# Optimization experiments

Measured on AMD Instinct MI355X. Metric: run time of the kernel, lower is better.

## Reference

```python
import jax, jax.numpy as jnp
import numpy as np

EPS = 1e-5

def batchnorm(x, gamma, beta):
    # training-mode BatchNorm1d: biased batch stats over axis 0
    mu = jnp.mean(x, axis=0)
    var = jnp.var(x, axis=0)
    return (x - mu) * jax.lax.rsqrt(var + EPS) * gamma + beta

def setup_inputs() -> dict:
    key = jax.random.key(0)
    ks = jax.random.split(key, 8)
    N, E, Hn, He = 50000, 800000, 128, 128
    node_emb = jax.random.normal(ks[0], (N, Hn), dtype=jnp.float32)
    edge_emb = jax.random.normal(ks[1], (E, He), dtype=jnp.float32)
    i = jax.random.randint(ks[2], (E,), 0, N, dtype=jnp.int64)
    fan_in = Hn + He
    W1 = jax.random.normal(ks[3], (fan_in, 2 * Hn), dtype=jnp.float32) / np.sqrt(fan_in)
    b1 = jnp.zeros((2 * Hn,), dtype=jnp.float32)
    gamma1 = jnp.ones((2 * Hn,), dtype=jnp.float32)
    beta1 = jnp.zeros((2 * Hn,), dtype=jnp.float32)
    gamma2 = jnp.ones((Hn,), dtype=jnp.float32)
    beta2 = jnp.zeros((Hn,), dtype=jnp.float32)
    return {"node_emb": node_emb, "edge_emb": edge_emb, "i": i,
            "W1": W1, "b1": b1, "gamma1": gamma1, "beta1": beta1,
            "gamma2": gamma2, "beta2": beta2}

def reference(node_emb, edge_emb, i, W1, b1, gamma1, beta1, gamma2, beta2):
    N = node_emb.shape[0]
    # gather + concat: [E, Hn+He]
    c1 = jnp.concatenate([node_emb[i], edge_emb], axis=1)
    # linear + BN: [E, 2*Hn]
    c1 = batchnorm(c1 @ W1 + b1, gamma1, beta1)
    c1_filter, c1_core = jnp.split(c1, 2, axis=1)
    msg = jax.nn.sigmoid(c1_filter) * jnp.tanh(c1_core)  # gated: [E, Hn]
    agg = jax.ops.segment_sum(msg, i, num_segments=N)     # scatter-add: [N, Hn]
    c1_emb = batchnorm(agg, gamma2, beta2)
    return jnp.tanh(node_emb + c1_emb)
```

## Files before the change

### kernel.cpp

```cpp
#include <hip/hip_runtime.h>
#include <hip/hip_bf16.h>

typedef __attribute__((ext_vector_type(8))) short short8;
typedef __attribute__((ext_vector_type(4))) float f32x4;

#define EPS 1e-5f

__device__ inline unsigned short bf16_rne(float x) {
    unsigned u = __float_as_uint(x);
    unsigned r = u + 0x7FFFu + ((u >> 16) & 1u);
    return (unsigned short)(r >> 16);
}

__device__ inline float sigmoidf_fast(float x) {
    return 1.0f / (1.0f + __expf(-x));
}

__device__ inline float tanhf_fast(float x) {
    float ax = fabsf(x);
    float e = __expf(-2.0f * ax);
    float t = (1.0f - e) / (1.0f + e);
    return copysignf(t, x);
}

__global__ void prep_w(const float* __restrict__ W1,
                       short* __restrict__ WhiT, short* __restrict__ WloT) {
    int n = blockIdx.x;
    int k = threadIdx.x;
    float x = W1[k * 256 + n];
    unsigned short hi = bf16_rne(x);
    float fh = __uint_as_float(((unsigned)hi) << 16);
    unsigned short lo = bf16_rne(x - fh);
    WhiT[n * 256 + k] = (short)hi;
    WloT[n * 256 + k] = (short)lo;
}

__global__ __launch_bounds__(256) void gemm_stats(
    const float* __restrict__ node_emb, const float* __restrict__ edge_emb,
    const int* __restrict__ idx,
    const short* __restrict__ WhiT, const short* __restrict__ WloT,
    const float* __restrict__ b1, float* __restrict__ h,
    float* __restrict__ sum1, float* __restrict__ sumsq1) {
    __shared__ __align__(16) short Ahi[64 * 128];
    __shared__ __align__(16) short Alo[64 * 128];

    const int tid = threadIdx.x;
    const int row0 = blockIdx.x * 64;
    const int r = tid >> 2;
    const int q = tid & 3;
    const size_t e = (size_t)row0 + r;
    const float* nodeptr = node_emb + (size_t)idx[e] * 128;
    const float* edgeptr = edge_emb + e * 128;

    const int lane = tid & 63;
    const int wid = tid >> 6;
    const int l15 = lane & 15;
    const int lg = lane >> 4;

    f32x4 acc[4][4];
#pragma unroll
    for (int a = 0; a < 4; ++a)
#pragma unroll
        for (int b = 0; b < 4; ++b) acc[a][b] = (f32x4){0.f, 0.f, 0.f, 0.f};

    const short* bbase_hi = WhiT + (wid * 64 + l15) * 256 + lg * 8;
    const short* bbase_lo = WloT + (wid * 64 + l15) * 256 + lg * 8;

#pragma unroll
    for (int ph = 0; ph < 2; ++ph) {
        const float* src = ph ? edgeptr : nodeptr;
        if (ph) __syncthreads();
#pragma unroll
        for (int cc = 0; cc < 4; ++cc) {
            const int c = q * 4 + cc;
            const int k0 = c * 8;
            float4 va = *(const float4*)(src + k0);
            float4 vb = *(const float4*)(src + k0 + 4);
            float vals[8] = {va.x, va.y, va.z, va.w, vb.x, vb.y, vb.z, vb.w};
            short8 vhi, vlo;
#pragma unroll
            for (int j = 0; j < 8; ++j) {
                unsigned short hb = bf16_rne(vals[j]);
                float fh = __uint_as_float(((unsigned)hb) << 16);
                unsigned short lb = bf16_rne(vals[j] - fh);
                vhi[j] = (short)hb;
                vlo[j] = (short)lb;
            }
            const int off = r * 128 + (c ^ (r & 7)) * 8;
            *(short8*)(Ahi + off) = vhi;
            *(short8*)(Alo + off) = vlo;
        }
        __syncthreads();

#pragma unroll
        for (int ks = 0; ks < 4; ++ks) {
            short8 ah[4], al[4];
#pragma unroll
            for (int mt = 0; mt < 4; ++mt) {
                const int row = mt * 16 + l15;
                const int off = row * 128 + ((ks * 4 + lg) ^ (row & 7)) * 8;
                ah[mt] = *(const short8*)(Ahi + off);
                al[mt] = *(const short8*)(Alo + off);
            }
            const int kglob = ph * 128 + ks * 32;
#pragma unroll
            for (int nt = 0; nt < 4; ++nt) {
                short8 bh = *(const short8*)(bbase_hi + nt * 16 * 256 + kglob);
                short8 bl = *(const short8*)(bbase_lo + nt * 16 * 256 + kglob);
#pragma unroll
                for (int mt = 0; mt < 4; ++mt) {
                    acc[mt][nt] = __builtin_amdgcn_mfma_f32_16x16x32_bf16(
                        ah[mt], bh, acc[mt][nt], 0, 0, 0);
                    acc[mt][nt] = __builtin_amdgcn_mfma_f32_16x16x32_bf16(
                        ah[mt], bl, acc[mt][nt], 0, 0, 0);
                    acc[mt][nt] = __builtin_amdgcn_mfma_f32_16x16x32_bf16(
                        al[mt], bh, acc[mt][nt], 0, 0, 0);
                }
            }
        }
    }

    const int colbase = wid * 64 + l15;
#pragma unroll
    for (int nt = 0; nt < 4; ++nt) {
        const int col = colbase + nt * 16;
        const float bv = b1[col];
        float s = 0.f, qq = 0.f;
#pragma unroll
        for (int mt = 0; mt < 4; ++mt) {
            const size_t rbase = (size_t)row0 + mt * 16 + lg * 4;
#pragma unroll
            for (int v = 0; v < 4; ++v) {
                float hv = acc[mt][nt][v] + bv;
                h[(rbase + v) * 256 + col] = hv;
                s += hv;
                qq += hv * hv;
            }
        }
        s += __shfl_xor(s, 16);
        s += __shfl_xor(s, 32);
        qq += __shfl_xor(qq, 16);
        qq += __shfl_xor(qq, 32);
        if (lg == 0) {
            atomicAdd(&sum1[col], s);
            atomicAdd(&sumsq1[col], qq);
        }
    }
}

__global__ void bn1_finalize(const float* __restrict__ sum1,
                             const float* __restrict__ sumsq1,
                             const float* __restrict__ gamma1,
                             const float* __restrict__ beta1,
                             float* __restrict__ s1t1, int E) {
    int c = threadIdx.x;
    float invE = 1.0f / (float)E;
    float mu = sum1[c] * invE;
    float var = sumsq1[c] * invE - mu * mu;
    float s = gamma1[c] * rsqrtf(var + EPS);
    s1t1[c] = s;
    s1t1[256 + c] = beta1[c] - mu * s;
}

__global__ void csr_hist(const int* __restrict__ idx, int* __restrict__ cnt,
                         int E) {
    int e = blockIdx.x * 256 + threadIdx.x;
    if (e < E) atomicAdd(&cnt[idx[e]], 1);
}

__global__ __launch_bounds__(1024) void csr_scan(const int* __restrict__ cnt,
                                                 int* __restrict__ offs, int N) {
    __shared__ int part[1024];
    const int t = threadIdx.x;
    const int CH = (N + 1023) / 1024;
    const int base = t * CH;
    int s = 0;
    for (int i = 0; i < CH; ++i)
        if (base + i < N) s += cnt[base + i];
    part[t] = s;
    __syncthreads();
    for (int d = 1; d < 1024; d <<= 1) {
        int v = (t >= d) ? part[t - d] : 0;
        __syncthreads();
        part[t] += v;
        __syncthreads();
    }
    int run = (t ? part[t - 1] : 0);
    for (int i = 0; i < CH; ++i) {
        int g = base + i;
        if (g < N) {
            offs[g] = run;
            run += cnt[g];
        }
    }
    if (t == 1023) offs[N] = run;
}

__global__ void csr_fill(const int* __restrict__ idx,
                         const int* __restrict__ offs, int* __restrict__ cursor,
                         int* __restrict__ elist, int E) {
    int e = blockIdx.x * 256 + threadIdx.x;
    if (e < E) {
        int n = idx[e];
        int p = atomicAdd(&cursor[n], 1);
        elist[offs[n] + p] = e;
    }
}

__global__ __launch_bounds__(256) void gate_gather(
    const float* __restrict__ h, const int* __restrict__ offs,
    const int* __restrict__ elist, const float* __restrict__ s1t1,
    float* __restrict__ agg, int N) {
    const int t = threadIdx.x;
    const int n = blockIdx.x * 8 + (t >> 5);
    const int c = (t & 31) * 4;
    const float4 sf = *(const float4*)(s1t1 + c);
    const float4 tf = *(const float4*)(s1t1 + 256 + c);
    const float4 sc = *(const float4*)(s1t1 + 128 + c);
    const float4 tc = *(const float4*)(s1t1 + 384 + c);
    const int j0 = offs[n];
    const int j1 = offs[n + 1];
    float a0 = 0.f, a1 = 0.f, a2 = 0.f, a3 = 0.f;
    for (int j = j0; j < j1; ++j) {
        const size_t e = (size_t)elist[j];
        const float4 hf = *(const float4*)(h + e * 256 + c);
        const float4 hc = *(const float4*)(h + e * 256 + 128 + c);
        a0 += sigmoidf_fast(hf.x * sf.x + tf.x) * tanhf_fast(hc.x * sc.x + tc.x);
        a1 += sigmoidf_fast(hf.y * sf.y + tf.y) * tanhf_fast(hc.y * sc.y + tc.y);
        a2 += sigmoidf_fast(hf.z * sf.z + tf.z) * tanhf_fast(hc.z * sc.z + tc.z);
        a3 += sigmoidf_fast(hf.w * sf.w + tf.w) * tanhf_fast(hc.w * sc.w + tc.w);
    }
    *(float4*)(agg + (size_t)n * 128 + c) = make_float4(a0, a1, a2, a3);
}

__global__ void bn2_stats(const float* __restrict__ agg, float* __restrict__ sum2,
                          float* __restrict__ sumsq2, int N) {
    const int gt = blockIdx.x * blockDim.x + threadIdx.x;
    const int c = (gt & 31) * 4;
    int r = gt >> 5;
    const int rstride = (gridDim.x * blockDim.x) >> 5;
    float s0 = 0, s1 = 0, s2 = 0, s3 = 0, q0 = 0, q1 = 0, q2 = 0, q3 = 0;
    for (; r < N; r += rstride) {
        float4 a = *(const float4*)(agg + (size_t)r * 128 + c);
        s0 += a.x; s1 += a.y; s2 += a.z; s3 += a.w;
        q0 += a.x * a.x; q1 += a.y * a.y; q2 += a.z * a.z; q3 += a.w * a.w;
    }
    atomicAdd(&sum2[c + 0], s0); atomicAdd(&sum2[c + 1], s1);
    atomicAdd(&sum2[c + 2], s2); atomicAdd(&sum2[c + 3], s3);
    atomicAdd(&sumsq2[c + 0], q0); atomicAdd(&sumsq2[c + 1], q1);
    atomicAdd(&sumsq2[c + 2], q2); atomicAdd(&sumsq2[c + 3], q3);
}

__global__ void finalize(const float* __restrict__ node,
                         const float* __restrict__ agg,
                         const float* __restrict__ sum2,
                         const float* __restrict__ sumsq2,
                         const float* __restrict__ gamma2,
                         const float* __restrict__ beta2,
                         float* __restrict__ out, int N) {
    const size_t gt = (size_t)blockIdx.x * blockDim.x + threadIdx.x;
    const size_t base = gt * 4;
    if (base >= (size_t)N * 128) return;
    const int c = (int)(base & 127);
    const float invN = 1.0f / (float)N;
    float4 a = *(const float4*)(agg + base);
    float4 x = *(const float4*)(node + base);
    float av[4] = {a.x, a.y, a.z, a.w};
    float xv[4] = {x.x, x.y, x.z, x.w};
    float4 o;
    float ov[4];
#pragma unroll
    for (int j = 0; j < 4; ++j) {
        float mu = sum2[c + j] * invN;
        float var = sumsq2[c + j] * invN - mu * mu;
        float s = gamma2[c + j] * rsqrtf(var + EPS);
        float t = beta2[c + j] - mu * s;
        ov[j] = tanhf_fast(xv[j] + av[j] * s + t);
    }
    o.x = ov[0]; o.y = ov[1]; o.z = ov[2]; o.w = ov[3];
    *(float4*)(out + base) = o;
}

extern "C" void kernel_launch(void* const* d_in, const int* in_sizes, int n_in,
                              void* d_out, int out_size, void* d_ws, size_t ws_size,
                              hipStream_t stream) {
    const float* node_emb = (const float*)d_in[0];
    const float* edge_emb = (const float*)d_in[1];
    const int* idx = (const int*)d_in[2];
    const float* W1 = (const float*)d_in[3];
    const float* b1 = (const float*)d_in[4];
    const float* gamma1 = (const float*)d_in[5];
    const float* beta1 = (const float*)d_in[6];
    const float* gamma2 = (const float*)d_in[7];
    const float* beta2 = (const float*)d_in[8];
    float* out = (float*)d_out;

    const int E = in_sizes[2];
    const int N = in_sizes[0] / 128;

    float* h = (float*)d_ws;
    float* agg = h + (size_t)E * 256;
    float* zbase = agg + (size_t)N * 128;
    float* sum1 = zbase;
    float* sumsq1 = sum1 + 256;
    float* s1t1 = sumsq1 + 256;
    float* sum2 = s1t1 + 512;
    float* sumsq2 = sum2 + 128;
    int* cnt = (int*)(sumsq2 + 128);
    int* cursor = cnt + N;
    int* offs = cursor + N;
    int* elist = offs + N + 8;
    short* WhiT = (short*)(elist + E);
    short* WloT = WhiT + 65536;

    const size_t zero_bytes = (size_t)(1280 + 2 * N) * 4;
    hipMemsetAsync(zbase, 0, zero_bytes, stream);

    prep_w<<<256, 256, 0, stream>>>(W1, WhiT, WloT);
    csr_hist<<<(E + 255) / 256, 256, 0, stream>>>(idx, cnt, E);
    csr_scan<<<1, 1024, 0, stream>>>(cnt, offs, N);
    csr_fill<<<(E + 255) / 256, 256, 0, stream>>>(idx, offs, cursor, elist, E);
    gemm_stats<<<E / 64, 256, 0, stream>>>(node_emb, edge_emb, idx, WhiT, WloT,
                                           b1, h, sum1, sumsq1);
    bn1_finalize<<<1, 256, 0, stream>>>(sum1, sumsq1, gamma1, beta1, s1t1, E);
    gate_gather<<<N / 8, 256, 0, stream>>>(h, offs, elist, s1t1, agg, N);
    bn2_stats<<<256, 256, 0, stream>>>(agg, sum2, sumsq2, N);
    finalize<<<(int)(((size_t)N * 128 / 4 + 255) / 256), 256, 0, stream>>>(
        node_emb, agg, sum2, sumsq2, gamma2, beta2, out, N);
}
```

Baseline: 1.727 ms.

## Widen GEMM block to 512 threads, prefetch both inputs, unroll gather loop

The GEMM kernel now runs 8 waves per 64-row tile, split 2x4 over rows and columns, so each wave holds half as many accumulators. Each thread issues its node and edge global loads at kernel start, before either compute phase, so the edge-phase load latency hides behind the node-phase MFMAs. The gate_gather loop is unrolled by four edges, giving more independent loads in flight per thread. The cost is more threads sharing the B-fragment global reads, since each B tile is now read by two waves, plus higher register pressure from the prefetched values.

```diff
diff --git a/kernel.cpp b/kernel.cpp
--- a/kernel.cpp
+++ b/kernel.cpp
@@ -21,6 +21,19 @@
     float e = __expf(-2.0f * ax);
     float t = (1.0f - e) / (1.0f + e);
     return copysignf(t, x);
+}
+
+__device__ inline void cvt8(const float4& a, const float4& b, short8& hi,
+                            short8& lo) {
+    float vals[8] = {a.x, a.y, a.z, a.w, b.x, b.y, b.z, b.w};
+#pragma unroll
+    for (int j = 0; j < 8; ++j) {
+        unsigned short hb = bf16_rne(vals[j]);
+        float fh = __uint_as_float(((unsigned)hb) << 16);
+        unsigned short lb = bf16_rne(vals[j] - fh);
+        hi[j] = (short)hb;
+        lo[j] = (short)lb;
+    }
 }
 
 __global__ void prep_w(const float* __restrict__ W1,
@@ -35,7 +48,32 @@
     WloT[n * 256 + k] = (short)lo;
 }
 
-__global__ __launch_bounds__(256) void gemm_stats(
+#define COMPUTE_PHASE(KBASE)                                                   \
+    _Pragma("unroll") for (int ks = 0; ks < 4; ++ks) {                         \
+        short8 ah[2], al[2];                                                   \
+        _Pragma("unroll") for (int mt = 0; mt < 2; ++mt) {                     \
+            const int row = wr * 32 + mt * 16 + l15;                           \
+            const int off = row * 128 + ((ks * 4 + lg) ^ (row & 7)) * 8;       \
+            ah[mt] = *(const short8*)(Ahi + off);                              \
+            al[mt] = *(const short8*)(Alo + off);                              \
+        }                                                                      \
+        _Pragma("unroll") for (int nt = 0; nt < 4; ++nt) {                     \
+            short8 bh =                                                        \
+                *(const short8*)(bbase_hi + nt * 16 * 256 + (KBASE) + ks * 32);\
+            short8 bl =                                                        \
+                *(const short8*)(bbase_lo + nt * 16 * 256 + (KBASE) + ks * 32);\
+            _Pragma("unroll") for (int mt = 0; mt < 2; ++mt) {                 \
+                acc[mt][nt] = __builtin_amdgcn_mfma_f32_16x16x32_bf16(         \
+                    ah[mt], bh, acc[mt][nt], 0, 0, 0);                         \
+                acc[mt][nt] = __builtin_amdgcn_mfma_f32_16x16x32_bf16(         \
+                    ah[mt], bl, acc[mt][nt], 0, 0, 0);                         \
+                acc[mt][nt] = __builtin_amdgcn_mfma_f32_16x16x32_bf16(         \
+                    al[mt], bh, acc[mt][nt], 0, 0, 0);                         \
+            }                                                                  \
+        }                                                                      \
+    }
+
+__global__ __launch_bounds__(512) void gemm_stats(
     const float* __restrict__ node_emb, const float* __restrict__ edge_emb,
     const int* __restrict__ idx,
     const short* __restrict__ WhiT, const short* __restrict__ WloT,
@@ -46,89 +84,76 @@
 
     const int tid = threadIdx.x;
     const int row0 = blockIdx.x * 64;
-    const int r = tid >> 2;
-    const int q = tid & 3;
+    const int r = tid >> 3;
+    const int q = tid & 7;
     const size_t e = (size_t)row0 + r;
-    const float* nodeptr = node_emb + (size_t)idx[e] * 128;
-    const float* edgeptr = edge_emb + e * 128;
+    const float* nodeptr = node_emb + (size_t)idx[e] * 128 + q * 16;
+    const float* edgeptr = edge_emb + e * 128 + q * 16;
+
+    const float4 n0 = *(const float4*)(nodeptr + 0);
+    const float4 n1 = *(const float4*)(nodeptr + 4);
+    const float4 n2 = *(const float4*)(nodeptr + 8);
+    const float4 n3 = *(const float4*)(nodeptr + 12);
+    const float4 e0 = *(const float4*)(edgeptr + 0);
+    const float4 e1 = *(const float4*)(edgeptr + 4);
+    const float4 e2 = *(const float4*)(edgeptr + 8);
+    const float4 e3 = *(const float4*)(edgeptr + 12);
 
     const int lane = tid & 63;
-    const int wid = tid >> 6;
+    const int w = tid >> 6;
+    const int wr = w & 1;
+    const int wc = w >> 1;
     const int l15 = lane & 15;
     const int lg = lane >> 4;
 
-    f32x4 acc[4][4];
-#pragma unroll
-    for (int a = 0; a < 4; ++a)
+    f32x4 acc[2][4];
+#pragma unroll
+    for (int a = 0; a < 2; ++a)
 #pragma unroll
         for (int b = 0; b < 4; ++b) acc[a][b] = (f32x4){0.f, 0.f, 0.f, 0.f};
 
-    const short* bbase_hi = WhiT + (wid * 64 + l15) * 256 + lg * 8;
-    const short* bbase_lo = WloT + (wid * 64 + l15) * 256 + lg * 8;
-
-#pragma unroll
-    for (int ph = 0; ph < 2; ++ph) {
-        const float* src = ph ? edgeptr : nodeptr;
-        if (ph) __syncthreads();
-#pragma unroll
-        for (int cc = 0; cc < 4; ++cc) {
-            const int c = q * 4 + cc;
-            const int k0 = c * 8;
-            float4 va = *(const float4*)(src + k0);
-            float4 vb = *(const float4*)(src + k0 + 4);
-            float vals[8] = {va.x, va.y, va.z, va.w, vb.x, vb.y, vb.z, vb.w};
-            short8 vhi, vlo;
-#pragma unroll
-            for (int j = 0; j < 8; ++j) {
-                unsigned short hb = bf16_rne(vals[j]);
-                float fh = __uint_as_float(((unsigned)hb) << 16);
-                unsigned short lb = bf16_rne(vals[j] - fh);
-                vhi[j] = (short)hb;
-                vlo[j] = (short)lb;
-            }
-            const int off = r * 128 + (c ^ (r & 7)) * 8;
-            *(short8*)(Ahi + off) = vhi;
-            *(short8*)(Alo + off) = vlo;
-        }
-        __syncthreads();
-
-#pragma unroll
-        for (int ks = 0; ks < 4; ++ks) {
-            short8 ah[4], al[4];
-#pragma unroll
-            for (int mt = 0; mt < 4; ++mt) {
-                const int row = mt * 16 + l15;
-                const int off = row * 128 + ((ks * 4 + lg) ^ (row & 7)) * 8;
-                ah[mt] = *(const short8*)(Ahi + off);
-                al[mt] = *(const short8*)(Alo + off);
-            }
-            const int kglob = ph * 128 + ks * 32;
-#pragma unroll
-            for (int nt = 0; nt < 4; ++nt) {
-                short8 bh = *(const short8*)(bbase_hi + nt * 16 * 256 + kglob);
-                short8 bl = *(const short8*)(bbase_lo + nt * 16 * 256 + kglob);
-#pragma unroll
-                for (int mt = 0; mt < 4; ++mt) {
-                    acc[mt][nt] = __builtin_amdgcn_mfma_f32_16x16x32_bf16(
-                        ah[mt], bh, acc[mt][nt], 0, 0, 0);
-                    acc[mt][nt] = __builtin_amdgcn_mfma_f32_16x16x32_bf16(
-                        ah[mt], bl, acc[mt][nt], 0, 0, 0);
-                    acc[mt][nt] = __builtin_amdgcn_mfma_f32_16x16x32_bf16(
-                        al[mt], bh, acc[mt][nt], 0, 0, 0);
-                }
-            }
-        }
-    }
-
-    const int colbase = wid * 64 + l15;
+    const short* bbase_hi = WhiT + (wc * 64 + l15) * 256 + lg * 8;
+    const short* bbase_lo = WloT + (wc * 64 + l15) * 256 + lg * 8;
+
+    const int off0 = r * 128 + ((2 * q) ^ (r & 7)) * 8;
+    const int off1 = r * 128 + ((2 * q + 1) ^ (r & 7)) * 8;
+
+    {
+        short8 h0, l0, h1, l1;
+        cvt8(n0, n1, h0, l0);
+        cvt8(n2, n3, h1, l1);
+        *(short8*)(Ahi + off0) = h0;
+        *(short8*)(Alo + off0) = l0;
+        *(short8*)(Ahi + off1) = h1;
+        *(short8*)(Alo + off1) = l1;
+    }
+    __syncthreads();
+
+    COMPUTE_PHASE(0)
+    __syncthreads();
+
+    {
+        short8 h0, l0, h1, l1;
+        cvt8(e0, e1, h0, l0);
+        cvt8(e2, e3, h1, l1);
+        *(short8*)(Ahi + off0) = h0;
+        *(short8*)(Alo + off0) = l0;
+        *(short8*)(Ahi + off1) = h1;
+        *(short8*)(Alo + off1) = l1;
+    }
+    __syncthreads();
+
+    COMPUTE_PHASE(128)
+
+    const int colbase = wc * 64 + l15;
 #pragma unroll
     for (int nt = 0; nt < 4; ++nt) {
         const int col = colbase + nt * 16;
         const float bv = b1[col];
         float s = 0.f, qq = 0.f;
 #pragma unroll
-        for (int mt = 0; mt < 4; ++mt) {
-            const size_t rbase = (size_t)row0 + mt * 16 + lg * 4;
+        for (int mt = 0; mt < 2; ++mt) {
+            const size_t rbase = (size_t)row0 + wr * 32 + mt * 16 + lg * 4;
 #pragma unroll
             for (int v = 0; v < 4; ++v) {
                 float hv = acc[mt][nt][v] + bv;
@@ -207,6 +232,16 @@
     }
 }
 
+__device__ inline void gate_acc(const float4& hf, const float4& hc,
+                                const float4& sf, const float4& tf,
+                                const float4& sc, const float4& tc, float& a0,
+                                float& a1, float& a2, float& a3) {
+    a0 += sigmoidf_fast(hf.x * sf.x + tf.x) * tanhf_fast(hc.x * sc.x + tc.x);
+    a1 += sigmoidf_fast(hf.y * sf.y + tf.y) * tanhf_fast(hc.y * sc.y + tc.y);
+    a2 += sigmoidf_fast(hf.z * sf.z + tf.z) * tanhf_fast(hc.z * sc.z + tc.z);
+    a3 += sigmoidf_fast(hf.w * sf.w + tf.w) * tanhf_fast(hc.w * sc.w + tc.w);
+}
+
 __global__ __launch_bounds__(256) void gate_gather(
     const float* __restrict__ h, const int* __restrict__ offs,
     const int* __restrict__ elist, const float* __restrict__ s1t1,
@@ -221,14 +256,30 @@
     const int j0 = offs[n];
     const int j1 = offs[n + 1];
     float a0 = 0.f, a1 = 0.f, a2 = 0.f, a3 = 0.f;
-    for (int j = j0; j < j1; ++j) {
+    int j = j0;
+    for (; j + 4 <= j1; j += 4) {
+        const size_t e0 = (size_t)elist[j + 0];
+        const size_t e1 = (size_t)elist[j + 1];
+        const size_t e2 = (size_t)elist[j + 2];
+        const size_t e3 = (size_t)elist[j + 3];
+        const float4 f0 = *(const float4*)(h + e0 * 256 + c);
+        const float4 c0 = *(const float4*)(h + e0 * 256 + 128 + c);
+        const float4 f1 = *(const float4*)(h + e1 * 256 + c);
+        const float4 c1 = *(const float4*)(h + e1 * 256 + 128 + c);
+        const float4 f2 = *(const float4*)(h + e2 * 256 + c);
+        const float4 c2 = *(const float4*)(h + e2 * 256 + 128 + c);
+        const float4 f3 = *(const float4*)(h + e3 * 256 + c);
+        const float4 c3 = *(const float4*)(h + e3 * 256 + 128 + c);
+        gate_acc(f0, c0, sf, tf, sc, tc, a0, a1, a2, a3);
+        gate_acc(f1, c1, sf, tf, sc, tc, a0, a1, a2, a3);
+        gate_acc(f2, c2, sf, tf, sc, tc, a0, a1, a2, a3);
+        gate_acc(f3, c3, sf, tf, sc, tc, a0, a1, a2, a3);
+    }
+    for (; j < j1; ++j) {
         const size_t e = (size_t)elist[j];
         const float4 hf = *(const float4*)(h + e * 256 + c);
         const float4 hc = *(const float4*)(h + e * 256 + 128 + c);
-        a0 += sigmoidf_fast(hf.x * sf.x + tf.x) * tanhf_fast(hc.x * sc.x + tc.x);
-        a1 += sigmoidf_fast(hf.y * sf.y + tf.y) * tanhf_fast(hc.y * sc.y + tc.y);
-        a2 += sigmoidf_fast(hf.z * sf.z + tf.z) * tanhf_fast(hc.z * sc.z + tc.z);
-        a3 += sigmoidf_fast(hf.w * sf.w + tf.w) * tanhf_fast(hc.w * sc.w + tc.w);
+        gate_acc(hf, hc, sf, tf, sc, tc, a0, a1, a2, a3);
     }
     *(float4*)(agg + (size_t)n * 128 + c) = make_float4(a0, a1, a2, a3);
 }
@@ -320,7 +371,7 @@
     csr_hist<<<(E + 255) / 256, 256, 0, stream>>>(idx, cnt, E);
     csr_scan<<<1, 1024, 0, stream>>>(cnt, offs, N);
     csr_fill<<<(E + 255) / 256, 256, 0, stream>>>(idx, offs, cursor, elist, E);
-    gemm_stats<<<E / 64, 256, 0, stream>>>(node_emb, edge_emb, idx, WhiT, WloT,
+    gemm_stats<<<E / 64, 512, 0, stream>>>(node_emb, edge_emb, idx, WhiT, WloT,
                                            b1, h, sum1, sumsq1);
     bn1_finalize<<<1, 256, 0, stream>>>(sum1, sumsq1, gamma1, beta1, s1t1, E);
     gate_gather<<<N / 8, 256, 0, stream>>>(h, offs, elist, s1t1, agg, N);
```

Result: slower. 2.016 ms (+16.7%).

## Store GEMM output as bf16 and split gated gather into scatter plus segment sum

Applied to the files above, without the earlier changes.

The pre-BN activation buffer is stored in bf16 instead of fp32, halving its write and read traffic, while batch statistics are still accumulated from the fp32 values. The gated message is computed per edge in edge order, reading h sequentially, and written to its CSR-sorted position. A separate segment-sum kernel then reduces contiguous rows. This replaces random row gathers with one scattered write, at the cost of an extra fp32 message buffer and reduced precision in h.

```diff
diff --git a/kernel.cpp b/kernel.cpp
--- a/kernel.cpp
+++ b/kernel.cpp
@@ -3,6 +3,7 @@
 
 typedef __attribute__((ext_vector_type(8))) short short8;
 typedef __attribute__((ext_vector_type(4))) float f32x4;
+typedef __attribute__((ext_vector_type(4))) unsigned short us4;
 
 #define EPS 1e-5f
 
@@ -10,6 +11,10 @@
     unsigned u = __float_as_uint(x);
     unsigned r = u + 0x7FFFu + ((u >> 16) & 1u);
     return (unsigned short)(r >> 16);
+}
+
+__device__ inline float b2f(unsigned short u) {
+    return __uint_as_float(((unsigned)u) << 16);
 }
 
 __device__ inline float sigmoidf_fast(float x) {
@@ -39,7 +44,7 @@
     const float* __restrict__ node_emb, const float* __restrict__ edge_emb,
     const int* __restrict__ idx,
     const short* __restrict__ WhiT, const short* __restrict__ WloT,
-    const float* __restrict__ b1, float* __restrict__ h,
+    const float* __restrict__ b1, unsigned short* __restrict__ hh,
     float* __restrict__ sum1, float* __restrict__ sumsq1) {
     __shared__ __align__(16) short Ahi[64 * 128];
     __shared__ __align__(16) short Alo[64 * 128];
@@ -132,7 +137,7 @@
 #pragma unroll
             for (int v = 0; v < 4; ++v) {
                 float hv = acc[mt][nt][v] + bv;
-                h[(rbase + v) * 256 + col] = hv;
+                hh[(rbase + v) * 256 + col] = bf16_rne(hv);
                 s += hv;
                 qq += hv * hv;
             }
@@ -198,37 +203,57 @@
 
 __global__ void csr_fill(const int* __restrict__ idx,
                          const int* __restrict__ offs, int* __restrict__ cursor,
-                         int* __restrict__ elist, int E) {
+                         int* __restrict__ epos, int E) {
     int e = blockIdx.x * 256 + threadIdx.x;
     if (e < E) {
         int n = idx[e];
         int p = atomicAdd(&cursor[n], 1);
-        elist[offs[n] + p] = e;
-    }
-}
-
-__global__ __launch_bounds__(256) void gate_gather(
-    const float* __restrict__ h, const int* __restrict__ offs,
-    const int* __restrict__ elist, const float* __restrict__ s1t1,
-    float* __restrict__ agg, int N) {
+        epos[e] = offs[n] + p;
+    }
+}
+
+__global__ __launch_bounds__(256) void gate_edge(
+    const unsigned short* __restrict__ hh, const int* __restrict__ epos,
+    const float* __restrict__ s1t1, float* __restrict__ msg, int E) {
     const int t = threadIdx.x;
-    const int n = blockIdx.x * 8 + (t >> 5);
+    const size_t e = (size_t)blockIdx.x * 8 + (t >> 5);
     const int c = (t & 31) * 4;
+    const us4 hf = *(const us4*)(hh + e * 256 + c);
+    const us4 hc = *(const us4*)(hh + e * 256 + 128 + c);
     const float4 sf = *(const float4*)(s1t1 + c);
     const float4 tf = *(const float4*)(s1t1 + 256 + c);
     const float4 sc = *(const float4*)(s1t1 + 128 + c);
     const float4 tc = *(const float4*)(s1t1 + 384 + c);
+    const int p = epos[e];
+    float4 m;
+    m.x = sigmoidf_fast(b2f(hf[0]) * sf.x + tf.x) * tanhf_fast(b2f(hc[0]) * sc.x + tc.x);
+    m.y = sigmoidf_fast(b2f(hf[1]) * sf.y + tf.y) * tanhf_fast(b2f(hc[1]) * sc.y + tc.y);
+    m.z = sigmoidf_fast(b2f(hf[2]) * sf.z + tf.z) * tanhf_fast(b2f(hc[2]) * sc.z + tc.z);
+    m.w = sigmoidf_fast(b2f(hf[3]) * sf.w + tf.w) * tanhf_fast(b2f(hc[3]) * sc.w + tc.w);
+    *(float4*)(msg + (size_t)p * 128 + c) = m;
+}
+
+__global__ __launch_bounds__(256) void seg_sum(const float* __restrict__ msg,
+                                               const int* __restrict__ offs,
+                                               float* __restrict__ agg, int N) {
+    const int t = threadIdx.x;
+    const int n = blockIdx.x * 8 + (t >> 5);
+    const int c = (t & 31) * 4;
     const int j0 = offs[n];
     const int j1 = offs[n + 1];
     float a0 = 0.f, a1 = 0.f, a2 = 0.f, a3 = 0.f;
-    for (int j = j0; j < j1; ++j) {
-        const size_t e = (size_t)elist[j];
-        const float4 hf = *(const float4*)(h + e * 256 + c);
-        const float4 hc = *(const float4*)(h + e * 256 + 128 + c);
-        a0 += sigmoidf_fast(hf.x * sf.x + tf.x) * tanhf_fast(hc.x * sc.x + tc.x);
-        a1 += sigmoidf_fast(hf.y * sf.y + tf.y) * tanhf_fast(hc.y * sc.y + tc.y);
-        a2 += sigmoidf_fast(hf.z * sf.z + tf.z) * tanhf_fast(hc.z * sc.z + tc.z);
-        a3 += sigmoidf_fast(hf.w * sf.w + tf.w) * tanhf_fast(hc.w * sc.w + tc.w);
+    int j = j0;
+    for (; j + 2 <= j1; j += 2) {
+        const float4 r0 = *(const float4*)(msg + (size_t)j * 128 + c);
+        const float4 r1 = *(const float4*)(msg + (size_t)(j + 1) * 128 + c);
+        a0 += r0.x + r1.x;
+        a1 += r0.y + r1.y;
+        a2 += r0.z + r1.z;
+        a3 += r0.w + r1.w;
+    }
+    if (j < j1) {
+        const float4 r0 = *(const float4*)(msg + (size_t)j * 128 + c);
+        a0 += r0.x; a1 += r0.y; a2 += r0.z; a3 += r0.w;
     }
     *(float4*)(agg + (size_t)n * 128 + c) = make_float4(a0, a1, a2, a3);
 }
@@ -298,8 +323,9 @@
     const int E = in_sizes[2];
     const int N = in_sizes[0] / 128;
 
-    float* h = (float*)d_ws;
-    float* agg = h + (size_t)E * 256;
+    unsigned short* hh = (unsigned short*)d_ws;
+    float* msg = (float*)((char*)d_ws + (size_t)E * 512);
+    float* agg = msg + (size_t)E * 128;
     float* zbase = agg + (size_t)N * 128;
     float* sum1 = zbase;
     float* sumsq1 = sum1 + 256;
@@ -309,8 +335,8 @@
     int* cnt = (int*)(sumsq2 + 128);
     int* cursor = cnt + N;
     int* offs = cursor + N;
-    int* elist = offs + N + 8;
-    short* WhiT = (short*)(elist + E);
+    int* epos = offs + N + 8;
+    short* WhiT = (short*)(epos + E);
     short* WloT = WhiT + 65536;
 
     const size_t zero_bytes = (size_t)(1280 + 2 * N) * 4;
@@ -319,11 +345,12 @@
     prep_w<<<256, 256, 0, stream>>>(W1, WhiT, WloT);
     csr_hist<<<(E + 255) / 256, 256, 0, stream>>>(idx, cnt, E);
     csr_scan<<<1, 1024, 0, stream>>>(cnt, offs, N);
-    csr_fill<<<(E + 255) / 256, 256, 0, stream>>>(idx, offs, cursor, elist, E);
+    csr_fill<<<(E + 255) / 256, 256, 0, stream>>>(idx, offs, cursor, epos, E);
     gemm_stats<<<E / 64, 256, 0, stream>>>(node_emb, edge_emb, idx, WhiT, WloT,
-                                           b1, h, sum1, sumsq1);
+                                           b1, hh, sum1, sumsq1);
     bn1_finalize<<<1, 256, 0, stream>>>(sum1, sumsq1, gamma1, beta1, s1t1, E);
-    gate_gather<<<N / 8, 256, 0, stream>>>(h, offs, elist, s1t1, agg, N);
+    gate_edge<<<E / 8, 256, 0, stream>>>(hh, epos, s1t1, msg, E);
+    seg_sum<<<N / 8, 256, 0, stream>>>(msg, offs, agg, N);
     bn2_stats<<<256, 256, 0, stream>>>(agg, sum2, sumsq2, N);
     finalize<<<(int)(((size_t)N * 128 / 4 + 255) / 256), 256, 0, stream>>>(
         node_emb, agg, sum2, sumsq2, gamma2, beta2, out, N);
```

New measurement: 1.717 ms. About the same (-0.6%).
